# Kernel tuning notes

Measured on AMD Instinct MI355X. Metric: run time of the kernel, lower is better.

The kernel has to match this reference:

```python
import jax, jax.numpy as jnp
import numpy as np

B, S, D = 8, 512, 512
H = 8
DPH = D // H
FFN = 2048
N_LAYERS = 4
K = 2048 * 8  # vocab_size * vq_vocab_size_factor
COMMIT = 0.25
LN_EPS = 1e-5
# replicates torch bug: scale = key.size(-1)//num_heads AFTER head split view
SCALE = DPH // H  # 64 // 8 = 8, attention is MULTIPLIED by this


def setup_inputs():
    key = jax.random.key(0)
    ks = jax.random.split(key, 12)
    init = lambda k, shape, s=0.02: (jax.random.normal(k, shape, jnp.float32) * s)
    inp = {
        'vec_inputs': jax.random.normal(ks[0], (B, S, D), jnp.float32),
        'Wq': init(ks[1], (N_LAYERS, D, D)), 'bq': jnp.zeros((N_LAYERS, D)),
        'Wk': init(ks[2], (N_LAYERS, D, D)), 'bk': jnp.zeros((N_LAYERS, D)),
        'Wv': init(ks[3], (N_LAYERS, D, D)), 'bv': jnp.zeros((N_LAYERS, D)),
        'Wo': init(ks[4], (N_LAYERS, D, D)), 'bo': jnp.zeros((N_LAYERS, D)),
        'ln1_g': jnp.ones((N_LAYERS, D)), 'ln1_b': jnp.zeros((N_LAYERS, D)),
        'W1': init(ks[5], (N_LAYERS, D, FFN)), 'b1': jnp.zeros((N_LAYERS, FFN)),
        'W2': init(ks[6], (N_LAYERS, FFN, D)), 'b2': jnp.zeros((N_LAYERS, D)),
        'ln2_g': jnp.ones((N_LAYERS, D)), 'ln2_b': jnp.zeros((N_LAYERS, D)),
        # VectorQuantizerEMA: embedding.weight.data.normal_()
        'codebook': jax.random.normal(ks[7], (K, D), jnp.float32),
    }
    return inp


def _layernorm(x, g, b):
    mu = jnp.mean(x, axis=-1, keepdims=True)
    var = jnp.mean((x - mu) ** 2, axis=-1, keepdims=True)
    return (x - mu) * jax.lax.rsqrt(var + LN_EPS) * g + b


def _encoder_layer(x, Wq, bq, Wk, bk, Wv, bv, Wo, bo, ln1_g, ln1_b, W1, b1, W2, b2, ln2_g, ln2_b):
    resid = x
    q = x @ Wq + bq  # [B,S,D]
    k = x @ Wk + bk
    v = x @ Wv + bv
    # faithful to torch .view(B*H, -1, dph): raw row-major reshape (NOT transpose split)
    q = q.reshape(B * H, S, DPH)
    k = k.reshape(B * H, S, DPH)
    v = v.reshape(B * H, S, DPH)
    att = jnp.einsum('bqd,bkd->bqk', q, k) * SCALE
    att = jax.nn.softmax(att, axis=-1)
    ctx = jnp.einsum('bqk,bkd->bqd', att, v).reshape(B, S, D)
    out = ctx @ Wo + bo
    out = _layernorm(resid + out, ln1_g, ln1_b)
    # position-wise FFN (Conv1d kernel 1 == Linear)
    ff = jax.nn.relu(out @ W1 + b1) @ W2 + b2
    out = _layernorm(out + ff, ln2_g, ln2_b)
    return out


def reference(vec_inputs, Wq, bq, Wk, bk, Wv, bv, Wo, bo, ln1_g, ln1_b,
              W1, b1, W2, b2, ln2_g, ln2_b, codebook):
    ze = vec_inputs
    for l in range(N_LAYERS):
        ze = _encoder_layer(ze, Wq[l], bq[l], Wk[l], bk[l], Wv[l], bv[l], Wo[l], bo[l],
                            ln1_g[l], ln1_b[l], W1[l], b1[l], W2[l], b2[l], ln2_g[l], ln2_b[l])
    # VectorQuantizerEMA forward (eval mode: no EMA updates)
    flat = ze.reshape(-1, D)  # [B*S, D]
    d = (jnp.sum(flat ** 2, axis=1, keepdims=True)
         + jnp.sum(codebook ** 2, axis=1)
         - 2.0 * flat @ codebook.T)  # [B*S, K]
    idx = jnp.argmin(d, axis=1)  # [B*S]
    quant = codebook[idx].reshape(ze.shape)
    e_latent = jnp.mean((jax.lax.stop_gradient(quant) - ze) ** 2)
    loss = COMMIT * e_latent
    zq = ze + jax.lax.stop_gradient(quant - ze)  # straight-through
    avg_probs = jnp.zeros((K,), jnp.float32).at[idx].add(1.0) / flat.shape[0]
    perplexity = jnp.exp(-jnp.sum(avg_probs * jnp.log(avg_probs + 1e-10)))
    return zq, idx.reshape(B, S), loss, perplexity
```

## Files before the change

### kernel.cpp

```cpp
#include <hip/hip_runtime.h>

#define MROWS 4096
#define DDIM  512
#define FFND  2048
#define NLAY  4
#define KCB   16384
#define LN_EPS 1e-5f

typedef unsigned short u16;
typedef _Float16 half8 __attribute__((ext_vector_type(8)));
typedef float f32x4 __attribute__((ext_vector_type(4)));

#define B_X    0ULL
#define B_Q    8388608ULL
#define B_K    16777216ULL
#define B_V    25165824ULL
#define B_CT   33554432ULL
#define B_TMP  41943040ULL
#define B_H    8388608ULL
#define B_CBH  8388608ULL
#define B_CBL  25165824ULL
#define B_ZEH  41943040ULL
#define B_ZEL  46137344ULL
#define B_ZN   50331648ULL
#define B_CN   50348032ULL
#define B_RL   50413568ULL
#define B_BEST 50429952ULL
#define B_HIST 50462720ULL
#define B_WT   50528256ULL

__device__ __forceinline__ void splitf16(float x, u16& h, u16& l) {
  _Float16 hh = (_Float16)x;
  float r = x - (float)hh;
  _Float16 ll = (_Float16)r;
  h = *(u16*)&hh; l = *(u16*)&ll;
}

__device__ __forceinline__ unsigned int fkey(float f) {
  unsigned int u = __float_as_uint(f);
  return (u & 0x80000000u) ? ~u : (u | 0x80000000u);
}

template<int EPI>
__device__ __forceinline__ void gemm64_body(const float* __restrict__ Af,
    const u16* __restrict__ Bhi, const u16* __restrict__ Blo,
    const float* __restrict__ bias, float* __restrict__ C, int Kd, int N) {
  __shared__ __align__(16) u16 As[2][2048];
  __shared__ __align__(16) u16 Bs[2][4096];
  const int t = threadIdx.x;
  const int w = t >> 6, l = t & 63;
  const int lr = l & 15, lg = l >> 4;
  const int m0 = blockIdx.y * 64, n0 = blockIdx.x * 128;

  f32x4 acc[4][2];
  const f32x4 zf = {0.f, 0.f, 0.f, 0.f};
#pragma unroll
  for (int mi = 0; mi < 4; ++mi)
#pragma unroll
    for (int ni = 0; ni < 2; ++ni) acc[mi][ni] = zf;

  for (int k0 = 0; k0 < Kd; k0 += 32) {
#pragma unroll
    for (int pl = 0; pl < 2; ++pl) {
      const u16* gp = pl ? Blo : Bhi;
      u16* lb = &Bs[pl][0];
#pragma unroll
      for (int i = 0; i < 2; ++i) {
        int ob = w * 2048 + i * 1024;
        int o = ob + l * 16;
        int r = o >> 6;
        int pc = (o >> 4) & 3;
        int c = pc ^ ((r + (r >> 2)) & 3);
        const u16* g = gp + (size_t)(n0 + r) * Kd + k0 + c * 8;
        __builtin_amdgcn_global_load_lds(
            (const __attribute__((address_space(1))) unsigned int*)(const void*)g,
            (__attribute__((address_space(3))) unsigned int*)(void*)(lb + (ob >> 1)), 16, 0, 0);
      }
    }
#pragma unroll
    for (int p = 0; p < 2; ++p) {
      int e = p * 256 + t;
      int r = e >> 3, kc = (e & 7) * 4;
      float4 a = *(const float4*)(Af + (size_t)(m0 + r) * Kd + k0 + kc);
      u16 h0, h1, h2, h3, q0, q1, q2, q3;
      splitf16(a.x, h0, q0); splitf16(a.y, h1, q1); splitf16(a.z, h2, q2); splitf16(a.w, h3, q3);
      int idx = r * 32 + ((((kc >> 3) ^ ((r + (r >> 2)) & 3))) << 3) + (kc & 7);
      *(uint2*)&As[0][idx] = make_uint2((unsigned)h0 | ((unsigned)h1 << 16), (unsigned)h2 | ((unsigned)h3 << 16));
      *(uint2*)&As[1][idx] = make_uint2((unsigned)q0 | ((unsigned)q1 << 16), (unsigned)q2 | ((unsigned)q3 << 16));
    }
    __syncthreads();
    half8 ah[4], al[4], bh2[2], bl2[2];
#pragma unroll
    for (int mi = 0; mi < 4; ++mi) {
      int r = mi * 16 + lr;
      int idx = r * 32 + ((lg ^ ((r + (r >> 2)) & 3)) << 3);
      ah[mi] = *(const half8*)&As[0][idx];
      al[mi] = *(const half8*)&As[1][idx];
    }
#pragma unroll
    for (int ni = 0; ni < 2; ++ni) {
      int r = w * 32 + ni * 16 + lr;
      int idx = r * 32 + ((lg ^ ((r + (r >> 2)) & 3)) << 3);
      bh2[ni] = *(const half8*)&Bs[0][idx];
      bl2[ni] = *(const half8*)&Bs[1][idx];
    }
#pragma unroll
    for (int mi = 0; mi < 4; ++mi)
#pragma unroll
      for (int ni = 0; ni < 2; ++ni) {
        acc[mi][ni] = __builtin_amdgcn_mfma_f32_16x16x32_f16(ah[mi], bh2[ni], acc[mi][ni], 0, 0, 0);
        acc[mi][ni] = __builtin_amdgcn_mfma_f32_16x16x32_f16(ah[mi], bl2[ni], acc[mi][ni], 0, 0, 0);
        acc[mi][ni] = __builtin_amdgcn_mfma_f32_16x16x32_f16(al[mi], bh2[ni], acc[mi][ni], 0, 0, 0);
      }
    __syncthreads();
  }

  float bv[2];
#pragma unroll
  for (int ni = 0; ni < 2; ++ni) bv[ni] = bias[n0 + w * 32 + ni * 16 + lr];
#pragma unroll
  for (int mi = 0; mi < 4; ++mi)
#pragma unroll
    for (int j = 0; j < 4; ++j) {
      int m = m0 + mi * 16 + lg * 4 + j;
#pragma unroll
      for (int ni = 0; ni < 2; ++ni) {
        int n = n0 + w * 32 + ni * 16 + lr;
        float o = acc[mi][ni][j] + bv[ni];
        if (EPI == 1) o = fmaxf(o, 0.f);
        C[(size_t)m * N + n] = o;
      }
    }
}

__global__ __launch_bounds__(256) void qkv_enc(const float* __restrict__ Af,
    const u16* __restrict__ wt, const float* __restrict__ bq, const float* __restrict__ bk,
    const float* __restrict__ bv_, float* __restrict__ Cq) {
  const int z = blockIdx.z;
  const u16* Bhi = wt + (size_t)z * 524288;
  const u16* Blo = Bhi + 262144;
  const float* bias = (z == 0) ? bq : (z == 1) ? bk : bv_;
  float* C = Cq + (size_t)z * 2097152;
  gemm64_body<0>(Af, Bhi, Blo, bias, C, 512, 512);
}

__global__ __launch_bounds__(256) void gemm_enc(const float* __restrict__ Af,
    const u16* __restrict__ Bhi, const u16* __restrict__ Blo,
    const float* __restrict__ bias, float* __restrict__ C, int Kd, int N) {
  gemm64_body<0>(Af, Bhi, Blo, bias, C, Kd, N);
}

template<int EPI>
__global__ __launch_bounds__(256) void gemm128(const float* __restrict__ Af,
    const u16* __restrict__ Bhi, const u16* __restrict__ Blo,
    const float* __restrict__ bias, float* __restrict__ C, int Kd, int N) {
  __shared__ __align__(16) u16 As[2][4096];
  __shared__ __align__(16) u16 Bs[2][4096];
  const int t = threadIdx.x;
  const int w = t >> 6, l = t & 63;
  const int lr = l & 15, lg = l >> 4;
  const int wr = w >> 1, wc = w & 1;
  const int m0 = blockIdx.y * 128, n0 = blockIdx.x * 128;

  f32x4 acc[4][4];
  const f32x4 zf = {0.f, 0.f, 0.f, 0.f};
#pragma unroll
  for (int mi = 0; mi < 4; ++mi)
#pragma unroll
    for (int ni = 0; ni < 4; ++ni) acc[mi][ni] = zf;

  for (int k0 = 0; k0 < Kd; k0 += 32) {
#pragma unroll
    for (int pl = 0; pl < 2; ++pl) {
      const u16* gp = pl ? Blo : Bhi;
      u16* lb = &Bs[pl][0];
#pragma unroll
      for (int i = 0; i < 2; ++i) {
        int ob = (w * 2 + i) * 1024;
        int o = ob + l * 16;
        int r = o >> 6;
        int c = ((o >> 4) & 3) ^ ((r + (r >> 2)) & 3);
        const u16* g = gp + (size_t)(n0 + r) * Kd + k0 + c * 8;
        __builtin_amdgcn_global_load_lds(
            (const __attribute__((address_space(1))) unsigned int*)(const void*)g,
            (__attribute__((address_space(3))) unsigned int*)(void*)(lb + (ob >> 1)), 16, 0, 0);
      }
    }
#pragma unroll
    for (int p = 0; p < 4; ++p) {
      int e = p * 256 + t;
      int r = e >> 3, kc = (e & 7) * 4;
      float4 a = *(const float4*)(Af + (size_t)(m0 + r) * Kd + k0 + kc);
      u16 h0, h1, h2, h3, q0, q1, q2, q3;
      splitf16(a.x, h0, q0); splitf16(a.y, h1, q1); splitf16(a.z, h2, q2); splitf16(a.w, h3, q3);
      int idx = r * 32 + ((((kc >> 3) ^ ((r + (r >> 2)) & 3))) << 3) + (kc & 7);
      *(uint2*)&As[0][idx] = make_uint2((unsigned)h0 | ((unsigned)h1 << 16), (unsigned)h2 | ((unsigned)h3 << 16));
      *(uint2*)&As[1][idx] = make_uint2((unsigned)q0 | ((unsigned)q1 << 16), (unsigned)q2 | ((unsigned)q3 << 16));
    }
    __syncthreads();
    half8 ah[4], al[4], bh4[4], bl4[4];
#pragma unroll
    for (int mi = 0; mi < 4; ++mi) {
      int r = wr * 64 + mi * 16 + lr;
      int idx = r * 32 + ((lg ^ ((r + (r >> 2)) & 3)) << 3);
      ah[mi] = *(const half8*)&As[0][idx];
      al[mi] = *(const half8*)&As[1][idx];
    }
#pragma unroll
    for (int ni = 0; ni < 4; ++ni) {
      int r = wc * 64 + ni * 16 + lr;
      int idx = r * 32 + ((lg ^ ((r + (r >> 2)) & 3)) << 3);
      bh4[ni] = *(const half8*)&Bs[0][idx];
      bl4[ni] = *(const half8*)&Bs[1][idx];
    }
#pragma unroll
    for (int mi = 0; mi < 4; ++mi)
#pragma unroll
      for (int ni = 0; ni < 4; ++ni) {
        acc[mi][ni] = __builtin_amdgcn_mfma_f32_16x16x32_f16(ah[mi], bh4[ni], acc[mi][ni], 0, 0, 0);
        acc[mi][ni] = __builtin_amdgcn_mfma_f32_16x16x32_f16(ah[mi], bl4[ni], acc[mi][ni], 0, 0, 0);
        acc[mi][ni] = __builtin_amdgcn_mfma_f32_16x16x32_f16(al[mi], bh4[ni], acc[mi][ni], 0, 0, 0);
      }
    __syncthreads();
  }

  float bv[4];
#pragma unroll
  for (int ni = 0; ni < 4; ++ni) bv[ni] = bias[n0 + wc * 64 + ni * 16 + lr];
#pragma unroll
  for (int mi = 0; mi < 4; ++mi)
#pragma unroll
    for (int j = 0; j < 4; ++j) {
      int m = m0 + wr * 64 + mi * 16 + lg * 4 + j;
#pragma unroll
      for (int ni = 0; ni < 4; ++ni) {
        int n = n0 + wc * 64 + ni * 16 + lr;
        float o = acc[mi][ni][j] + bv[ni];
        if (EPI == 1) o = fmaxf(o, 0.f);
        C[(size_t)m * N + n] = o;
      }
    }
}

__global__ __launch_bounds__(512) void attn_mfma(const float* __restrict__ Q,
    const float* __restrict__ Kx, const float* __restrict__ V, float* __restrict__ O) {
  __shared__ __align__(16) u16 Ks[2][4608];
  __shared__ __align__(16) u16 Ps[2][9216];
  __shared__ __align__(16) u16 Vt[2][4608];
  const int t = threadIdx.x;
  const int w = t >> 6, l = t & 63;
  const int lr = l & 15, lg = l >> 4;
  const int bh = blockIdx.y;
  const int q0 = blockIdx.x * 128;
  const float* Qb = Q + ((size_t)bh * 512 + q0) * 64;
  const float* Kb = Kx + (size_t)bh * 512 * 64;
  const float* Vb = V + (size_t)bh * 512 * 64;

  const int srow = t >> 4, sc4 = (t & 15) * 4;

  half8 qh[2], qlo[2];
#pragma unroll
  for (int ks = 0; ks < 2; ++ks) {
    const float* p = Qb + (size_t)(w * 16 + lr) * 64 + ks * 32 + lg * 8;
    float4 f0 = *(const float4*)p;
    float4 f1 = *(const float4*)(p + 4);
    float v8[8] = {f0.x, f0.y, f0.z, f0.w, f1.x, f1.y, f1.z, f1.w};
#pragma unroll
    for (int j = 0; j < 8; ++j) {
      _Float16 hh = (_Float16)v8[j];
      float r = v8[j] - (float)hh;
      qh[ks][j] = hh;
      qlo[ks][j] = (_Float16)r;
    }
  }

  float mrun[4] = {-1e30f, -1e30f, -1e30f, -1e30f};
  float lrun[4] = {0.f, 0.f, 0.f, 0.f};
  f32x4 o[4];
  const f32x4 zf = {0.f, 0.f, 0.f, 0.f};
#pragma unroll
  for (int dn = 0; dn < 4; ++dn) o[dn] = zf;

  float4 kreg[2], vreg[2];
#pragma unroll
  for (int i = 0; i < 2; ++i) {
    int row = i * 32 + srow;
    kreg[i] = *(const float4*)(Kb + (size_t)row * 64 + sc4);
    vreg[i] = *(const float4*)(Vb + (size_t)row * 64 + sc4);
  }

#pragma unroll 1
  for (int kc = 0; kc < 8; ++kc) {
    __syncthreads();
#pragma unroll
    for (int i = 0; i < 2; ++i) {
      int row = i * 32 + srow;
      u16 h0, h1, h2, h3, l0, l1, l2, l3;
      splitf16(kreg[i].x, h0, l0); splitf16(kreg[i].y, h1, l1);
      splitf16(kreg[i].z, h2, l2); splitf16(kreg[i].w, h3, l3);
      *(uint2*)&Ks[0][row * 72 + sc4] = make_uint2((unsigned)h0 | ((unsigned)h1 << 16), (unsigned)h2 | ((unsigned)h3 << 16));
      *(uint2*)&Ks[1][row * 72 + sc4] = make_uint2((unsigned)l0 | ((unsigned)l1 << 16), (unsigned)l2 | ((unsigned)l3 << 16));
      u16 vh[4], vl[4];
      splitf16(vreg[i].x, vh[0], vl[0]); splitf16(vreg[i].y, vh[1], vl[1]);
      splitf16(vreg[i].z, vh[2], vl[2]); splitf16(vreg[i].w, vh[3], vl[3]);
#pragma unroll
      for (int ii = 0; ii < 4; ++ii) {
        Vt[0][(sc4 + ii) * 72 + row] = vh[ii];
        Vt[1][(sc4 + ii) * 72 + row] = vl[ii];
      }
    }
    __syncthreads();
    if (kc < 7) {
#pragma unroll
      for (int i = 0; i < 2; ++i) {
        int row = i * 32 + srow;
        kreg[i] = *(const float4*)(Kb + (size_t)((kc + 1) * 64 + row) * 64 + sc4);
        vreg[i] = *(const float4*)(Vb + (size_t)((kc + 1) * 64 + row) * 64 + sc4);
      }
    }
    f32x4 sa[4];
#pragma unroll
    for (int ni = 0; ni < 4; ++ni) sa[ni] = zf;
    __builtin_amdgcn_s_setprio(1);
#pragma unroll
    for (int ks = 0; ks < 2; ++ks) {
#pragma unroll
      for (int ni = 0; ni < 4; ++ni) {
        half8 kh = *(const half8*)&Ks[0][(ni * 16 + lr) * 72 + ks * 32 + lg * 8];
        half8 klo = *(const half8*)&Ks[1][(ni * 16 + lr) * 72 + ks * 32 + lg * 8];
        sa[ni] = __builtin_amdgcn_mfma_f32_16x16x32_f16(qh[ks], kh, sa[ni], 0, 0, 0);
        sa[ni] = __builtin_amdgcn_mfma_f32_16x16x32_f16(qh[ks], klo, sa[ni], 0, 0, 0);
        sa[ni] = __builtin_amdgcn_mfma_f32_16x16x32_f16(qlo[ks], kh, sa[ni], 0, 0, 0);
      }
    }
    __builtin_amdgcn_s_setprio(0);
#pragma unroll
    for (int j = 0; j < 4; ++j) {
      float sv[4];
#pragma unroll
      for (int ni = 0; ni < 4; ++ni) sv[ni] = sa[ni][j] * 8.f;
      float mx = fmaxf(fmaxf(sv[0], sv[1]), fmaxf(sv[2], sv[3]));
#pragma unroll
      for (int off = 8; off; off >>= 1) mx = fmaxf(mx, __shfl_xor(mx, off, 16));
      float mnew = fmaxf(mrun[j], mx);
      float fac = expf(mrun[j] - mnew);
      float ps = 0.f;
#pragma unroll
      for (int ni = 0; ni < 4; ++ni) {
        float p = expf(sv[ni] - mnew);
        ps += p;
        u16 ph_, pl_;
        splitf16(p, ph_, pl_);
        Ps[0][(w * 16 + lg * 4 + j) * 72 + ni * 16 + lr] = ph_;
        Ps[1][(w * 16 + lg * 4 + j) * 72 + ni * 16 + lr] = pl_;
      }
#pragma unroll
      for (int off = 8; off; off >>= 1) ps += __shfl_xor(ps, off, 16);
      lrun[j] = lrun[j] * fac + ps;
      mrun[j] = mnew;
#pragma unroll
      for (int dn = 0; dn < 4; ++dn) o[dn][j] *= fac;
    }
    __builtin_amdgcn_s_setprio(1);
#pragma unroll
    for (int ks = 0; ks < 2; ++ks) {
      half8 ph8 = *(const half8*)&Ps[0][(w * 16 + lr) * 72 + ks * 32 + lg * 8];
      half8 pl8 = *(const half8*)&Ps[1][(w * 16 + lr) * 72 + ks * 32 + lg * 8];
#pragma unroll
      for (int dn = 0; dn < 4; ++dn) {
        half8 vh8 = *(const half8*)&Vt[0][(dn * 16 + lr) * 72 + ks * 32 + lg * 8];
        half8 vl8 = *(const half8*)&Vt[1][(dn * 16 + lr) * 72 + ks * 32 + lg * 8];
        o[dn] = __builtin_amdgcn_mfma_f32_16x16x32_f16(ph8, vh8, o[dn], 0, 0, 0);
        o[dn] = __builtin_amdgcn_mfma_f32_16x16x32_f16(ph8, vl8, o[dn], 0, 0, 0);
        o[dn] = __builtin_amdgcn_mfma_f32_16x16x32_f16(pl8, vh8, o[dn], 0, 0, 0);
      }
    }
    __builtin_amdgcn_s_setprio(0);
  }
  float inv[4];
#pragma unroll
  for (int j = 0; j < 4; ++j) inv[j] = 1.f / lrun[j];
  float* Ob = O + ((size_t)bh * 512 + q0) * 64;
#pragma unroll
  for (int dn = 0; dn < 4; ++dn)
#pragma unroll
    for (int j = 0; j < 4; ++j)
      Ob[(size_t)(w * 16 + lg * 4 + j) * 64 + dn * 16 + lr] = o[dn][j] * inv[j];
}

__global__ __launch_bounds__(1024) void vq256(
    const u16* __restrict__ Ahi, const u16* __restrict__ Alo,
    const u16* __restrict__ Bhi, const u16* __restrict__ Blo,
    const float* __restrict__ zn, const float* __restrict__ cn,
    unsigned long long* __restrict__ best) {
  __shared__ __align__(16) u16 As[2][2][8192];
  __shared__ __align__(16) u16 Bs[2][2][8192];
  const int t = threadIdx.x;
  const int w = t >> 6, l = t & 63;
  const int lr = l & 15, lg = l >> 4;
  const int wr = w >> 2, wc = w & 3;
  const int f = blockIdx.x;
  const int xcd = f & 7, pos = f >> 3;
  const int ml = pos & 15;
  const int nl = pos >> 4;
  const int n0 = (xcd * 8 + nl) * 256;
  const int m0 = ml * 256;

  f32x4 acc[4][4];
  const f32x4 zf = {0.f, 0.f, 0.f, 0.f};
#pragma unroll
  for (int mi = 0; mi < 4; ++mi)
#pragma unroll
    for (int ni = 0; ni < 4; ++ni) acc[mi][ni] = zf;

  const int s_ob = w * 1024;
  int s_r, s_c;
  {
    int o = s_ob + l * 16;
    s_r = o >> 6;
    s_c = ((o >> 4) & 3) ^ ((s_r + (s_r >> 2)) & 3);
  }

#define VQ_STAGE(buf, k0)                                                               \
  {                                                                                     \
    size_t ea = (size_t)(m0 + s_r) * 512 + (k0) + s_c * 8;                              \
    size_t eb = (size_t)(n0 + s_r) * 512 + (k0) + s_c * 8;                              \
    __builtin_amdgcn_global_load_lds(                                                   \
        (const __attribute__((address_space(1))) unsigned int*)(const void*)(Ahi + ea), \
        (__attribute__((address_space(3))) unsigned int*)(void*)(&As[buf][0][s_ob >> 1]), 16, 0, 0); \
    __builtin_amdgcn_global_load_lds(                                                   \
        (const __attribute__((address_space(1))) unsigned int*)(const void*)(Alo + ea), \
        (__attribute__((address_space(3))) unsigned int*)(void*)(&As[buf][1][s_ob >> 1]), 16, 0, 0); \
    __builtin_amdgcn_global_load_lds(                                                   \
        (const __attribute__((address_space(1))) unsigned int*)(const void*)(Bhi + eb), \
        (__attribute__((address_space(3))) unsigned int*)(void*)(&Bs[buf][0][s_ob >> 1]), 16, 0, 0); \
    __builtin_amdgcn_global_load_lds(                                                   \
        (const __attribute__((address_space(1))) unsigned int*)(const void*)(Blo + eb), \
        (__attribute__((address_space(3))) unsigned int*)(void*)(&Bs[buf][1][s_ob >> 1]), 16, 0, 0); \
  }

#define VQ_COMPUTE(buf)                                                                 \
  {                                                                                     \
    half8 bh[4], bl[4];                                                                 \
    _Pragma("unroll")                                                                   \
    for (int ni = 0; ni < 4; ++ni) {                                                    \
      int r = wc * 64 + ni * 16 + lr;                                                   \
      int idx = r * 32 + ((lg ^ ((r + (r >> 2)) & 3)) << 3);                            \
      bh[ni] = *(const half8*)&Bs[buf][0][idx];                                         \
      bl[ni] = *(const half8*)&Bs[buf][1][idx];                                         \
    }                                                                                   \
    _Pragma("unroll")                                                                   \
    for (int mi = 0; mi < 4; ++mi) {                                                    \
      int r = wr * 64 + mi * 16 + lr;                                                   \
      int idx = r * 32 + ((lg ^ ((r + (r >> 2)) & 3)) << 3);                            \
      half8 ah = *(const half8*)&As[buf][0][idx];                                       \
      half8 al = *(const half8*)&As[buf][1][idx];                                       \
      _Pragma("unroll")                                                                 \
      for (int ni = 0; ni < 4; ++ni) {                                                  \
        acc[mi][ni] = __builtin_amdgcn_mfma_f32_16x16x32_f16(ah, bh[ni], acc[mi][ni], 0, 0, 0); \
        acc[mi][ni] = __builtin_amdgcn_mfma_f32_16x16x32_f16(ah, bl[ni], acc[mi][ni], 0, 0, 0); \
        acc[mi][ni] = __builtin_amdgcn_mfma_f32_16x16x32_f16(al, bh[ni], acc[mi][ni], 0, 0, 0); \
      }                                                                                 \
    }                                                                                   \
  }

  VQ_STAGE(0, 0);
  asm volatile("s_waitcnt vmcnt(0)" ::: "memory");
  __builtin_amdgcn_s_barrier();
  int cur = 0;
#pragma unroll 1
  for (int ks = 0; ks < 16; ++ks) {
    if (ks < 15) VQ_STAGE(cur ^ 1, (ks + 1) * 32);
    VQ_COMPUTE(cur);
    asm volatile("s_waitcnt vmcnt(0)" ::: "memory");
    __builtin_amdgcn_s_barrier();
    cur ^= 1;
  }

  float cnv[4];
#pragma unroll
  for (int ni = 0; ni < 4; ++ni) cnv[ni] = cn[n0 + wc * 64 + ni * 16 + lr];
#pragma unroll
  for (int mi = 0; mi < 4; ++mi)
#pragma unroll
    for (int j = 0; j < 4; ++j) {
      int m = m0 + wr * 64 + mi * 16 + lg * 4 + j;
      float zr = zn[m];
      float db = 3.4e38f; int jb = 0;
#pragma unroll
      for (int ni = 0; ni < 4; ++ni) {
        float dd = zr + cnv[ni] - 2.f * acc[mi][ni][j];
        int nn = n0 + wc * 64 + ni * 16 + lr;
        if (dd < db) { db = dd; jb = nn; }
      }
      unsigned long long key = ((unsigned long long)fkey(db) << 32) | (unsigned int)jb;
#pragma unroll
      for (int off = 8; off; off >>= 1) {
        unsigned long long o = __shfl_xor(key, off, 16);
        if (o < key) key = o;
      }
      if (lr == 0) atomicMin(best + m, key);
    }
#undef VQ_STAGE
#undef VQ_COMPUTE
}

__global__ __launch_bounds__(256) void wcvt_layer(const float* __restrict__ Wq,
    const float* __restrict__ Wk, const float* __restrict__ Wv, const float* __restrict__ Wo,
    const float* __restrict__ W1, const float* __restrict__ W2, u16* __restrict__ wt) {
  __shared__ float Ls[64][68];
  const int T = blockIdx.x, t = threadIdx.x;
  const float* src; u16 *dh, *dl; int K, N, kt, nt;
  if (T < 256) {
    int mat = T >> 6, tt = T & 63;
    src = (mat == 0) ? Wq : (mat == 1) ? Wk : (mat == 2) ? Wv : Wo;
    dh = wt + (size_t)mat * 524288; dl = dh + 262144;
    K = 512; N = 512; kt = tt >> 3; nt = tt & 7;
  } else if (T < 512) {
    int tt = T - 256; src = W1; dh = wt + 2097152; dl = dh + 1048576;
    K = 512; N = 2048; kt = tt >> 5; nt = tt & 31;
  } else {
    int tt = T - 512; src = W2; dh = wt + 4194304; dl = dh + 1048576;
    K = 2048; N = 512; kt = tt >> 3; nt = tt & 7;
  }
  const int k0 = kt * 64, n0 = nt * 64;
#pragma unroll
  for (int p = 0; p < 4; ++p) {
    int e = p * 256 + t;
    int kr = e >> 4, nc = (e & 15) * 4;
    *(float4*)&Ls[kr][nc] = *(const float4*)(src + (size_t)(k0 + kr) * N + n0 + nc);
  }
  __syncthreads();
  {
    int n = t >> 2, kc = (t & 3) * 16;
    unsigned hw[8], lw[8];
#pragma unroll
    for (int i = 0; i < 8; ++i) {
      u16 ha, la, hb, lb;
      splitf16(Ls[kc + 2 * i][n], ha, la);
      splitf16(Ls[kc + 2 * i + 1][n], hb, lb);
      hw[i] = (unsigned)ha | ((unsigned)hb << 16);
      lw[i] = (unsigned)la | ((unsigned)lb << 16);
    }
    size_t o = (size_t)(n0 + n) * K + k0 + kc;
    *(uint4*)&dh[o] = make_uint4(hw[0], hw[1], hw[2], hw[3]);
    *(uint4*)&dh[o + 8] = make_uint4(hw[4], hw[5], hw[6], hw[7]);
    *(uint4*)&dl[o] = make_uint4(lw[0], lw[1], lw[2], lw[3]);
    *(uint4*)&dl[o + 8] = make_uint4(lw[4], lw[5], lw[6], lw[7]);
  }
}

__global__ __launch_bounds__(128) void zcvt_kernel(const float* __restrict__ src,
    u16* __restrict__ hi, u16* __restrict__ lo, float* __restrict__ nrm) {
  __shared__ float red[2];
  const int row = blockIdx.x, t = threadIdx.x;
  const float4 a = *(const float4*)(src + (size_t)row * 512 + t * 4);
  u16 h0, h1, h2, h3, q0, q1, q2, q3;
  splitf16(a.x, h0, q0); splitf16(a.y, h1, q1); splitf16(a.z, h2, q2); splitf16(a.w, h3, q3);
  *(uint2*)&hi[(size_t)row * 512 + t * 4] = make_uint2((unsigned)h0 | ((unsigned)h1 << 16), (unsigned)h2 | ((unsigned)h3 << 16));
  *(uint2*)&lo[(size_t)row * 512 + t * 4] = make_uint2((unsigned)q0 | ((unsigned)q1 << 16), (unsigned)q2 | ((unsigned)q3 << 16));
  float s = a.x * a.x + a.y * a.y + a.z * a.z + a.w * a.w;
#pragma unroll
  for (int off = 32; off; off >>= 1) s += __shfl_xor(s, off, 64);
  if ((t & 63) == 0) red[t >> 6] = s;
  __syncthreads();
  if (t == 0) nrm[row] = red[0] + red[1];
}

__global__ __launch_bounds__(128) void ln_kernel(const float* __restrict__ A,
    const float* __restrict__ Dl, const float* __restrict__ g,
    const float* __restrict__ bb, float* __restrict__ out) {
  __shared__ float red[2];
  const int row = blockIdx.x, t = threadIdx.x;
  const float4 a = *(const float4*)(A + (size_t)row * 512 + t * 4);
  const float4 d = *(const float4*)(Dl + (size_t)row * 512 + t * 4);
  float v0 = a.x + d.x, v1 = a.y + d.y, v2 = a.z + d.z, v3 = a.w + d.w;
  float s = v0 + v1 + v2 + v3;
#pragma unroll
  for (int off = 32; off; off >>= 1) s += __shfl_xor(s, off, 64);
  if ((t & 63) == 0) red[t >> 6] = s;
  __syncthreads();
  const float mu = (red[0] + red[1]) * (1.f / 512.f);
  const float w0 = v0 - mu, w1 = v1 - mu, w2 = v2 - mu, w3 = v3 - mu;
  float q = w0 * w0 + w1 * w1 + w2 * w2 + w3 * w3;
  __syncthreads();
#pragma unroll
  for (int off = 32; off; off >>= 1) q += __shfl_xor(q, off, 64);
  if ((t & 63) == 0) red[t >> 6] = q;
  __syncthreads();
  const float rs = rsqrtf((red[0] + red[1]) * (1.f / 512.f) + LN_EPS);
  const float4 gv = *(const float4*)(g + t * 4);
  const float4 bv = *(const float4*)(bb + t * 4);
  *(float4*)(out + (size_t)row * 512 + t * 4) =
      make_float4(w0 * rs * gv.x + bv.x, w1 * rs * gv.y + bv.y, w2 * rs * gv.z + bv.z, w3 * rs * gv.w + bv.w);
}

__global__ __launch_bounds__(128) void gather_kernel(const unsigned long long* __restrict__ best,
    const float* __restrict__ Cb, const float* __restrict__ Ze, float* __restrict__ zq,
    float* __restrict__ oidx, float* __restrict__ rloss, int* __restrict__ hist) {
  __shared__ float red[2];
  const int row = blockIdx.x, t = threadIdx.x;
  const int idx = (int)(best[row] & 0xFFFFFFFFULL);
  const float4 c = *(const float4*)(Cb + (size_t)idx * 512 + t * 4);
  const float4 z = *(const float4*)(Ze + (size_t)row * 512 + t * 4);
  *(float4*)(zq + (size_t)row * 512 + t * 4) = c;
  const float d0 = c.x - z.x, d1 = c.y - z.y, d2 = c.z - z.z, d3 = c.w - z.w;
  float s = d0 * d0 + d1 * d1 + d2 * d2 + d3 * d3;
#pragma unroll
  for (int off = 32; off; off >>= 1) s += __shfl_xor(s, off, 64);
  if ((t & 63) == 0) red[t >> 6] = s;
  __syncthreads();
  if (t == 0) {
    rloss[row] = red[0] + red[1];
    oidx[row] = (float)idx;
    atomicAdd(hist + idx, 1);
  }
}

__global__ __launch_bounds__(256) void fin_kernel(const float* __restrict__ rloss,
    const int* __restrict__ hist, float* __restrict__ oloss, float* __restrict__ oppl) {
  __shared__ float red[4];
  const int t = threadIdx.x;
  float s = 0.f;
  for (int i = t; i < 4096; i += 256) s += rloss[i];
#pragma unroll
  for (int off = 32; off; off >>= 1) s += __shfl_xor(s, off, 64);
  if ((t & 63) == 0) red[t >> 6] = s;
  __syncthreads();
  if (t == 0) oloss[0] = 0.25f * (red[0] + red[1] + red[2] + red[3]) * (1.f / 2097152.f);
  float e = 0.f;
  for (int i = t; i < KCB; i += 256) {
    float p = (float)hist[i] * (1.f / 4096.f);
    e += p * logf(p + 1e-10f);
  }
#pragma unroll
  for (int off = 32; off; off >>= 1) e += __shfl_xor(e, off, 64);
  __syncthreads();
  if ((t & 63) == 0) red[t >> 6] = e;
  __syncthreads();
  if (t == 0) oppl[0] = expf(-(red[0] + red[1] + red[2] + red[3]));
}

extern "C" void kernel_launch(void* const* d_in, const int* in_sizes, int n_in,
                              void* d_out, int out_size, void* d_ws, size_t ws_size,
                              hipStream_t stream) {
  const float* vec  = (const float*)d_in[0];
  const float* Wq   = (const float*)d_in[1];
  const float* bq   = (const float*)d_in[2];
  const float* Wk   = (const float*)d_in[3];
  const float* bk   = (const float*)d_in[4];
  const float* Wv   = (const float*)d_in[5];
  const float* bv   = (const float*)d_in[6];
  const float* Wo   = (const float*)d_in[7];
  const float* bo   = (const float*)d_in[8];
  const float* l1g  = (const float*)d_in[9];
  const float* l1b  = (const float*)d_in[10];
  const float* W1   = (const float*)d_in[11];
  const float* b1   = (const float*)d_in[12];
  const float* W2   = (const float*)d_in[13];
  const float* b2   = (const float*)d_in[14];
  const float* l2g  = (const float*)d_in[15];
  const float* l2b  = (const float*)d_in[16];
  const float* cb   = (const float*)d_in[17];

  char* wsb = (char*)d_ws;
  float* x   = (float*)(wsb + B_X);
  float* q   = (float*)(wsb + B_Q);
  float* k   = (float*)(wsb + B_K);
  float* v   = (float*)(wsb + B_V);
  float* ctx = (float*)(wsb + B_CT);
  float* tmp = (float*)(wsb + B_TMP);
  float* h   = (float*)(wsb + B_H);
  u16* cbh = (u16*)(wsb + B_CBH);
  u16* cbl = (u16*)(wsb + B_CBL);
  u16* zeh = (u16*)(wsb + B_ZEH);
  u16* zel = (u16*)(wsb + B_ZEL);
  float* zn = (float*)(wsb + B_ZN);
  float* cn = (float*)(wsb + B_CN);
  float* rl = (float*)(wsb + B_RL);
  unsigned long long* best = (unsigned long long*)(wsb + B_BEST);
  int* hist = (int*)(wsb + B_HIST);
  u16* wt = (u16*)(wsb + B_WT);
  u16* wto_h = wt + 1572864;      u16* wto_l = wt + 1835008;
  u16* wt1_h = wt + 2097152;      u16* wt1_l = wt + 3145728;
  u16* wt2_h = wt + 4194304;      u16* wt2_l = wt + 5242880;

  float* zq   = (float*)d_out;
  float* oidx = (float*)d_out + 2097152;
  float* olos = (float*)d_out + 2097152 + 4096;
  float* oppl = olos + 1;

  const dim3 gQkv(4, 64, 3);
  const dim3 gProj(4, 64);
  const dim3 gFfn1(16, 32);
  const dim3 gAttn(4, 64);

  for (int l = 0; l < NLAY; ++l) {
    const float* xin = l ? (const float*)x : vec;
    const size_t wo = (size_t)l * DDIM * DDIM;
    wcvt_layer<<<768, 256, 0, stream>>>(Wq + wo, Wk + wo, Wv + wo, Wo + wo,
        W1 + (size_t)l * DDIM * FFND, W2 + (size_t)l * FFND * DDIM, wt);
    qkv_enc<<<gQkv, 256, 0, stream>>>(xin, wt, bq + l * DDIM, bk + l * DDIM, bv + l * DDIM, q);
    attn_mfma<<<gAttn, 512, 0, stream>>>(q, k, v, ctx);
    gemm_enc<<<gProj, 256, 0, stream>>>(ctx, wto_h, wto_l, bo + l * DDIM, tmp, DDIM, DDIM);
    ln_kernel<<<MROWS, 128, 0, stream>>>(xin, tmp, l1g + l * DDIM, l1b + l * DDIM, x);
    gemm128<1><<<gFfn1, 256, 0, stream>>>(x, wt1_h, wt1_l, b1 + l * FFND, h, DDIM, FFND);
    gemm_enc<<<gProj, 256, 0, stream>>>(h, wt2_h, wt2_l, b2 + l * DDIM, tmp, FFND, DDIM);
    ln_kernel<<<MROWS, 128, 0, stream>>>(x, tmp, l2g + l * DDIM, l2b + l * DDIM, x);
  }

  zcvt_kernel<<<MROWS, 128, 0, stream>>>(x, zeh, zel, zn);
  zcvt_kernel<<<KCB, 128, 0, stream>>>(cb, cbh, cbl, cn);
  hipMemsetAsync(best, 0xFF, 4096 * 8, stream);
  hipMemsetAsync(hist, 0, KCB * 4, stream);
  vq256<<<1024, 1024, 0, stream>>>(zeh, zel, cbh, cbl, zn, cn, best);
  gather_kernel<<<MROWS, 128, 0, stream>>>(best, cb, x, zq, oidx, rl, hist);
  fin_kernel<<<1, 256, 0, stream>>>(rl, hist, olos, oppl);
}
```

Baseline: 1.033 ms.

## Split-K the output and FFN2 projections and fold partial sums into layernorm

Replaces the single-pass 64x128-tile projection GEMMs (Wo and W2) with a split-K variant that launches twice as many blocks, each covering half the reduction dimension and writing its own partial buffer. The layernorm kernel now reads both partials plus the bias and sums them with the residual, so no separate reduction pass is needed. This raises block count for the 512-wide outputs to improve CU occupancy, at the cost of an extra full-size fp32 write and read per GEMM.

Result: faster. 901.8 us (median of 2 runs) (-12.7%).

```diff
diff --git a/kernel.cpp b/kernel.cpp
--- a/kernel.cpp
+++ b/kernel.cpp
@@ -28,6 +28,7 @@
 #define B_BEST 50429952ULL
 #define B_HIST 50462720ULL
 #define B_WT   50528256ULL
+#define B_TMP2 63111168ULL
 
 __device__ __forceinline__ void splitf16(float x, u16& h, u16& l) {
   _Float16 hh = (_Float16)x;
@@ -144,10 +145,94 @@
   gemm64_body<0>(Af, Bhi, Blo, bias, C, 512, 512);
 }
 
-__global__ __launch_bounds__(256) void gemm_enc(const float* __restrict__ Af,
+__global__ __launch_bounds__(256) void gemm_splitk(const float* __restrict__ Af,
     const u16* __restrict__ Bhi, const u16* __restrict__ Blo,
-    const float* __restrict__ bias, float* __restrict__ C, int Kd, int N) {
-  gemm64_body<0>(Af, Bhi, Blo, bias, C, Kd, N);
+    float* __restrict__ C0, float* __restrict__ C1, int Kd, int N) {
+  __shared__ __align__(16) u16 As[2][2048];
+  __shared__ __align__(16) u16 Bs[2][4096];
+  const int t = threadIdx.x;
+  const int w = t >> 6, l = t & 63;
+  const int lr = l & 15, lg = l >> 4;
+  const int m0 = blockIdx.y * 64, n0 = blockIdx.x * 128;
+  const int z = blockIdx.z;
+  const int koff = z * (Kd >> 1);
+  const int kend = koff + (Kd >> 1);
+  float* C = z ? C1 : C0;
+
+  f32x4 acc[4][2];
+  const f32x4 zf = {0.f, 0.f, 0.f, 0.f};
+#pragma unroll
+  for (int mi = 0; mi < 4; ++mi)
+#pragma unroll
+    for (int ni = 0; ni < 2; ++ni) acc[mi][ni] = zf;
+
+  for (int k0 = koff; k0 < kend; k0 += 32) {
+#pragma unroll
+    for (int pl = 0; pl < 2; ++pl) {
+      const u16* gp = pl ? Blo : Bhi;
+      u16* lb = &Bs[pl][0];
+#pragma unroll
+      for (int i = 0; i < 2; ++i) {
+        int ob = w * 2048 + i * 1024;
+        int o = ob + l * 16;
+        int r = o >> 6;
+        int pc = (o >> 4) & 3;
+        int c = pc ^ ((r + (r >> 2)) & 3);
+        const u16* g = gp + (size_t)(n0 + r) * Kd + k0 + c * 8;
+        __builtin_amdgcn_global_load_lds(
+            (const __attribute__((address_space(1))) unsigned int*)(const void*)g,
+            (__attribute__((address_space(3))) unsigned int*)(void*)(lb + (ob >> 1)), 16, 0, 0);
+      }
+    }
+#pragma unroll
+    for (int p = 0; p < 2; ++p) {
+      int e = p * 256 + t;
+      int r = e >> 3, kc = (e & 7) * 4;
+      float4 a = *(const float4*)(Af + (size_t)(m0 + r) * Kd + k0 + kc);
+      u16 h0, h1, h2, h3, q0, q1, q2, q3;
+      splitf16(a.x, h0, q0); splitf16(a.y, h1, q1); splitf16(a.z, h2, q2); splitf16(a.w, h3, q3);
+      int idx = r * 32 + ((((kc >> 3) ^ ((r + (r >> 2)) & 3))) << 3) + (kc & 7);
+      *(uint2*)&As[0][idx] = make_uint2((unsigned)h0 | ((unsigned)h1 << 16), (unsigned)h2 | ((unsigned)h3 << 16));
+      *(uint2*)&As[1][idx] = make_uint2((unsigned)q0 | ((unsigned)q1 << 16), (unsigned)q2 | ((unsigned)q3 << 16));
+    }
+    __syncthreads();
+    half8 ah[4], al[4], bh2[2], bl2[2];
+#pragma unroll
+    for (int mi = 0; mi < 4; ++mi) {
+      int r = mi * 16 + lr;
+      int idx = r * 32 + ((lg ^ ((r + (r >> 2)) & 3)) << 3);
+      ah[mi] = *(const half8*)&As[0][idx];
+      al[mi] = *(const half8*)&As[1][idx];
+    }
+#pragma unroll
+    for (int ni = 0; ni < 2; ++ni) {
+      int r = w * 32 + ni * 16 + lr;
+      int idx = r * 32 + ((lg ^ ((r + (r >> 2)) & 3)) << 3);
+      bh2[ni] = *(const half8*)&Bs[0][idx];
+      bl2[ni] = *(const half8*)&Bs[1][idx];
+    }
+#pragma unroll
+    for (int mi = 0; mi < 4; ++mi)
+#pragma unroll
+      for (int ni = 0; ni < 2; ++ni) {
+        acc[mi][ni] = __builtin_amdgcn_mfma_f32_16x16x32_f16(ah[mi], bh2[ni], acc[mi][ni], 0, 0, 0);
+        acc[mi][ni] = __builtin_amdgcn_mfma_f32_16x16x32_f16(ah[mi], bl2[ni], acc[mi][ni], 0, 0, 0);
+        acc[mi][ni] = __builtin_amdgcn_mfma_f32_16x16x32_f16(al[mi], bh2[ni], acc[mi][ni], 0, 0, 0);
+      }
+    __syncthreads();
+  }
+
+#pragma unroll
+  for (int mi = 0; mi < 4; ++mi)
+#pragma unroll
+    for (int j = 0; j < 4; ++j) {
+      int m = m0 + mi * 16 + lg * 4 + j;
+#pragma unroll
+      for (int ni = 0; ni < 2; ++ni) {
+        int n = n0 + w * 32 + ni * 16 + lr;
+        C[(size_t)m * N + n] = acc[mi][ni][j];
+      }
+    }
 }
 
 template<int EPI>
@@ -567,14 +652,17 @@
   if (t == 0) nrm[row] = red[0] + red[1];
 }
 
-__global__ __launch_bounds__(128) void ln_kernel(const float* __restrict__ A,
-    const float* __restrict__ Dl, const float* __restrict__ g,
-    const float* __restrict__ bb, float* __restrict__ out) {
+__global__ __launch_bounds__(128) void ln3_kernel(const float* __restrict__ A,
+    const float* __restrict__ D1, const float* __restrict__ D2, const float* __restrict__ gb,
+    const float* __restrict__ g, const float* __restrict__ bb, float* __restrict__ out) {
   __shared__ float red[2];
   const int row = blockIdx.x, t = threadIdx.x;
-  const float4 a = *(const float4*)(A + (size_t)row * 512 + t * 4);
-  const float4 d = *(const float4*)(Dl + (size_t)row * 512 + t * 4);
-  float v0 = a.x + d.x, v1 = a.y + d.y, v2 = a.z + d.z, v3 = a.w + d.w;
+  const float4 a  = *(const float4*)(A  + (size_t)row * 512 + t * 4);
+  const float4 d1 = *(const float4*)(D1 + (size_t)row * 512 + t * 4);
+  const float4 d2 = *(const float4*)(D2 + (size_t)row * 512 + t * 4);
+  const float4 gv2 = *(const float4*)(gb + t * 4);
+  float v0 = a.x + d1.x + d2.x + gv2.x, v1 = a.y + d1.y + d2.y + gv2.y;
+  float v2 = a.z + d1.z + d2.z + gv2.z, v3 = a.w + d1.w + d2.w + gv2.w;
   float s = v0 + v1 + v2 + v3;
 #pragma unroll
   for (int off = 32; off; off >>= 1) s += __shfl_xor(s, off, 64);
@@ -664,13 +752,14 @@
   const float* cb   = (const float*)d_in[17];
 
   char* wsb = (char*)d_ws;
-  float* x   = (float*)(wsb + B_X);
-  float* q   = (float*)(wsb + B_Q);
-  float* k   = (float*)(wsb + B_K);
-  float* v   = (float*)(wsb + B_V);
-  float* ctx = (float*)(wsb + B_CT);
-  float* tmp = (float*)(wsb + B_TMP);
-  float* h   = (float*)(wsb + B_H);
+  float* x    = (float*)(wsb + B_X);
+  float* q    = (float*)(wsb + B_Q);
+  float* k    = (float*)(wsb + B_K);
+  float* v    = (float*)(wsb + B_V);
+  float* ctx  = (float*)(wsb + B_CT);
+  float* tmp  = (float*)(wsb + B_TMP);
+  float* tmp2 = (float*)(wsb + B_TMP2);
+  float* h    = (float*)(wsb + B_H);
   u16* cbh = (u16*)(wsb + B_CBH);
   u16* cbl = (u16*)(wsb + B_CBL);
   u16* zeh = (u16*)(wsb + B_ZEH);
@@ -691,7 +780,7 @@
   float* oppl = olos + 1;
 
   const dim3 gQkv(4, 64, 3);
-  const dim3 gProj(4, 64);
+  const dim3 gSplit(4, 64, 2);
   const dim3 gFfn1(16, 32);
   const dim3 gAttn(4, 64);
 
@@ -702,11 +791,13 @@
         W1 + (size_t)l * DDIM * FFND, W2 + (size_t)l * FFND * DDIM, wt);
     qkv_enc<<<gQkv, 256, 0, stream>>>(xin, wt, bq + l * DDIM, bk + l * DDIM, bv + l * DDIM, q);
     attn_mfma<<<gAttn, 512, 0, stream>>>(q, k, v, ctx);
-    gemm_enc<<<gProj, 256, 0, stream>>>(ctx, wto_h, wto_l, bo + l * DDIM, tmp, DDIM, DDIM);
-    ln_kernel<<<MROWS, 128, 0, stream>>>(xin, tmp, l1g + l * DDIM, l1b + l * DDIM, x);
+    gemm_splitk<<<gSplit, 256, 0, stream>>>(ctx, wto_h, wto_l, tmp, tmp2, DDIM, DDIM);
+    ln3_kernel<<<MROWS, 128, 0, stream>>>(xin, tmp, tmp2, bo + l * DDIM,
+        l1g + l * DDIM, l1b + l * DDIM, x);
     gemm128<1><<<gFfn1, 256, 0, stream>>>(x, wt1_h, wt1_l, b1 + l * FFND, h, DDIM, FFND);
-    gemm_enc<<<gProj, 256, 0, stream>>>(h, wt2_h, wt2_l, b2 + l * DDIM, tmp, FFND, DDIM);
-    ln_kernel<<<MROWS, 128, 0, stream>>>(x, tmp, l2g + l * DDIM, l2b + l * DDIM, x);
+    gemm_splitk<<<gSplit, 256, 0, stream>>>(h, wt2_h, wt2_l, tmp, tmp2, FFND, DDIM);
+    ln3_kernel<<<MROWS, 128, 0, stream>>>(x, tmp, tmp2, b2 + l * DDIM,
+        l2g + l * DDIM, l2b + l * DDIM, x);
   }
 
   zcvt_kernel<<<MROWS, 128, 0, stream>>>(x, zeh, zel, zn);
```

## Split-K the 512-wide GEMMs and fuse partial-sum reduction into consumers

Applied to the files above, without the earlier changes.

The QKV, output-projection and FFN2 GEMMs are split into two K-halves via blockIdx.z, doubling the number of blocks on the 64x128-tile launches. Each half writes its partial sums to its own buffer. The two partials plus the bias are summed inside the attention kernel (for Q/K/V) and inside a new LayerNorm variant (for the projections), so no separate reduction pass is needed. The aim is better CU occupancy on the small grids, paid for with extra partial-buffer writes and reads, and with the attention output aliasing the Q2 buffer.

Result: faster. 939.7 us (-9.0%).

```diff
diff --git a/kernel.cpp b/kernel.cpp
--- a/kernel.cpp
+++ b/kernel.cpp
@@ -28,6 +28,7 @@
 #define B_BEST 50429952ULL
 #define B_HIST 50462720ULL
 #define B_WT   50528256ULL
+#define B_TMP2 63111168ULL
 
 __device__ __forceinline__ void splitf16(float x, u16& h, u16& l) {
   _Float16 hh = (_Float16)x;
@@ -41,10 +42,9 @@
   return (u & 0x80000000u) ? ~u : (u | 0x80000000u);
 }
 
-template<int EPI>
-__device__ __forceinline__ void gemm64_body(const float* __restrict__ Af,
+__device__ __forceinline__ void gemm64_nk_body(const float* __restrict__ Af,
     const u16* __restrict__ Bhi, const u16* __restrict__ Blo,
-    const float* __restrict__ bias, float* __restrict__ C, int Kd, int N) {
+    float* __restrict__ C, int Kd, int N, int koff, int kend) {
   __shared__ __align__(16) u16 As[2][2048];
   __shared__ __align__(16) u16 Bs[2][4096];
   const int t = threadIdx.x;
@@ -59,7 +59,7 @@
 #pragma unroll
     for (int ni = 0; ni < 2; ++ni) acc[mi][ni] = zf;
 
-  for (int k0 = 0; k0 < Kd; k0 += 32) {
+  for (int k0 = koff; k0 < kend; k0 += 32) {
 #pragma unroll
     for (int pl = 0; pl < 2; ++pl) {
       const u16* gp = pl ? Blo : Bhi;
@@ -115,9 +115,6 @@
     __syncthreads();
   }
 
-  float bv[2];
-#pragma unroll
-  for (int ni = 0; ni < 2; ++ni) bv[ni] = bias[n0 + w * 32 + ni * 16 + lr];
 #pragma unroll
   for (int mi = 0; mi < 4; ++mi)
 #pragma unroll
@@ -126,28 +123,29 @@
 #pragma unroll
       for (int ni = 0; ni < 2; ++ni) {
         int n = n0 + w * 32 + ni * 16 + lr;
-        float o = acc[mi][ni][j] + bv[ni];
-        if (EPI == 1) o = fmaxf(o, 0.f);
-        C[(size_t)m * N + n] = o;
-      }
-    }
-}
-
-__global__ __launch_bounds__(256) void qkv_enc(const float* __restrict__ Af,
-    const u16* __restrict__ wt, const float* __restrict__ bq, const float* __restrict__ bk,
-    const float* __restrict__ bv_, float* __restrict__ Cq) {
+        C[(size_t)m * N + n] = acc[mi][ni][j];
+      }
+    }
+}
+
+__global__ __launch_bounds__(256) void gemm_splitk(const float* __restrict__ Af,
+    const u16* __restrict__ Bhi, const u16* __restrict__ Blo,
+    float* __restrict__ C0, float* __restrict__ C1, int Kd, int N) {
   const int z = blockIdx.z;
-  const u16* Bhi = wt + (size_t)z * 524288;
+  gemm64_nk_body(Af, Bhi, Blo, z ? C1 : C0, Kd, N, z * (Kd >> 1), (z + 1) * (Kd >> 1));
+}
+
+__global__ __launch_bounds__(256) void qkv_splitk(const float* __restrict__ Af,
+    const u16* __restrict__ wt,
+    float* __restrict__ q1, float* __restrict__ k1, float* __restrict__ v1,
+    float* __restrict__ q2, float* __restrict__ k2, float* __restrict__ v2) {
+  const int z = blockIdx.z;
+  const int mat = z >> 1, half = z & 1;
+  const u16* Bhi = wt + (size_t)mat * 524288;
   const u16* Blo = Bhi + 262144;
-  const float* bias = (z == 0) ? bq : (z == 1) ? bk : bv_;
-  float* C = Cq + (size_t)z * 2097152;
-  gemm64_body<0>(Af, Bhi, Blo, bias, C, 512, 512);
-}
-
-__global__ __launch_bounds__(256) void gemm_enc(const float* __restrict__ Af,
-    const u16* __restrict__ Bhi, const u16* __restrict__ Blo,
-    const float* __restrict__ bias, float* __restrict__ C, int Kd, int N) {
-  gemm64_body<0>(Af, Bhi, Blo, bias, C, Kd, N);
+  float* C = half ? ((mat == 0) ? q2 : (mat == 1) ? k2 : v2)
+                  : ((mat == 0) ? q1 : (mat == 1) ? k1 : v1);
+  gemm64_nk_body(Af, Bhi, Blo, C, 512, 512, half * 256, half * 256 + 256);
 }
 
 template<int EPI>
@@ -242,8 +240,12 @@
     }
 }
 
-__global__ __launch_bounds__(512) void attn_mfma(const float* __restrict__ Q,
-    const float* __restrict__ Kx, const float* __restrict__ V, float* __restrict__ O) {
+__global__ __launch_bounds__(512) void attn_mfma(
+    const float* __restrict__ Q1, const float* __restrict__ Q2,
+    const float* __restrict__ K1, const float* __restrict__ K2,
+    const float* __restrict__ V1, const float* __restrict__ V2,
+    const float* __restrict__ bq, const float* __restrict__ bk, const float* __restrict__ bv_,
+    float* __restrict__ O) {
   __shared__ __align__(16) u16 Ks[2][4608];
   __shared__ __align__(16) u16 Ps[2][9216];
   __shared__ __align__(16) u16 Vt[2][4608];
@@ -252,19 +254,32 @@
   const int lr = l & 15, lg = l >> 4;
   const int bh = blockIdx.y;
   const int q0 = blockIdx.x * 128;
-  const float* Qb = Q + ((size_t)bh * 512 + q0) * 64;
-  const float* Kb = Kx + (size_t)bh * 512 * 64;
-  const float* Vb = V + (size_t)bh * 512 * 64;
+  const size_t poff = ((size_t)bh * 512 + q0) * 64;
+  const size_t koffb = (size_t)bh * 512 * 64;
+  const float* Qb1 = Q1 + poff;
+  const float* Qb2 = Q2 + poff;
+  const float* Kb1 = K1 + koffb;
+  const float* Kb2 = K2 + koffb;
+  const float* Vb1 = V1 + koffb;
+  const float* Vb2 = V2 + koffb;
 
   const int srow = t >> 4, sc4 = (t & 15) * 4;
+  const float4 bk4 = *(const float4*)(bk + ((srow & 7) << 6) + sc4);
+  const float4 bv4 = *(const float4*)(bv_ + ((srow & 7) << 6) + sc4);
 
   half8 qh[2], qlo[2];
 #pragma unroll
   for (int ks = 0; ks < 2; ++ks) {
-    const float* p = Qb + (size_t)(w * 16 + lr) * 64 + ks * 32 + lg * 8;
-    float4 f0 = *(const float4*)p;
-    float4 f1 = *(const float4*)(p + 4);
-    float v8[8] = {f0.x, f0.y, f0.z, f0.w, f1.x, f1.y, f1.z, f1.w};
+    const size_t ro = (size_t)(w * 16 + lr) * 64 + ks * 32 + lg * 8;
+    float4 f0 = *(const float4*)(Qb1 + ro);
+    float4 f1 = *(const float4*)(Qb1 + ro + 4);
+    float4 g0 = *(const float4*)(Qb2 + ro);
+    float4 g1 = *(const float4*)(Qb2 + ro + 4);
+    const float* bp = bq + ((lr & 7) << 6) + ks * 32 + lg * 8;
+    float4 b0 = *(const float4*)bp;
+    float4 b1 = *(const float4*)(bp + 4);
+    float v8[8] = {f0.x + g0.x + b0.x, f0.y + g0.y + b0.y, f0.z + g0.z + b0.z, f0.w + g0.w + b0.w,
+                   f1.x + g1.x + b1.x, f1.y + g1.y + b1.y, f1.z + g1.z + b1.z, f1.w + g1.w + b1.w};
 #pragma unroll
     for (int j = 0; j < 8; ++j) {
       _Float16 hh = (_Float16)v8[j];
@@ -281,12 +296,14 @@
 #pragma unroll
   for (int dn = 0; dn < 4; ++dn) o[dn] = zf;
 
-  float4 kreg[2], vreg[2];
+  float4 kra[2], krb[2], vra[2], vrb[2];
 #pragma unroll
   for (int i = 0; i < 2; ++i) {
-    int row = i * 32 + srow;
-    kreg[i] = *(const float4*)(Kb + (size_t)row * 64 + sc4);
-    vreg[i] = *(const float4*)(Vb + (size_t)row * 64 + sc4);
+    size_t ro = (size_t)(i * 32 + srow) * 64 + sc4;
+    kra[i] = *(const float4*)(Kb1 + ro);
+    krb[i] = *(const float4*)(Kb2 + ro);
+    vra[i] = *(const float4*)(Vb1 + ro);
+    vrb[i] = *(const float4*)(Vb2 + ro);
   }
 
 #pragma unroll 1
@@ -295,14 +312,17 @@
 #pragma unroll
     for (int i = 0; i < 2; ++i) {
       int row = i * 32 + srow;
+      float kx = kra[i].x + krb[i].x + bk4.x, ky = kra[i].y + krb[i].y + bk4.y;
+      float kz = kra[i].z + krb[i].z + bk4.z, kw = kra[i].w + krb[i].w + bk4.w;
       u16 h0, h1, h2, h3, l0, l1, l2, l3;
-      splitf16(kreg[i].x, h0, l0); splitf16(kreg[i].y, h1, l1);
-      splitf16(kreg[i].z, h2, l2); splitf16(kreg[i].w, h3, l3);
+      splitf16(kx, h0, l0); splitf16(ky, h1, l1); splitf16(kz, h2, l2); splitf16(kw, h3, l3);
       *(uint2*)&Ks[0][row * 72 + sc4] = make_uint2((unsigned)h0 | ((unsigned)h1 << 16), (unsigned)h2 | ((unsigned)h3 << 16));
       *(uint2*)&Ks[1][row * 72 + sc4] = make_uint2((unsigned)l0 | ((unsigned)l1 << 16), (unsigned)l2 | ((unsigned)l3 << 16));
+      float vx = vra[i].x + vrb[i].x + bv4.x, vy = vra[i].y + vrb[i].y + bv4.y;
+      float vz = vra[i].z + vrb[i].z + bv4.z, vw = vra[i].w + vrb[i].w + bv4.w;
       u16 vh[4], vl[4];
-      splitf16(vreg[i].x, vh[0], vl[0]); splitf16(vreg[i].y, vh[1], vl[1]);
-      splitf16(vreg[i].z, vh[2], vl[2]); splitf16(vreg[i].w, vh[3], vl[3]);
+      splitf16(vx, vh[0], vl[0]); splitf16(vy, vh[1], vl[1]);
+      splitf16(vz, vh[2], vl[2]); splitf16(vw, vh[3], vl[3]);
 #pragma unroll
       for (int ii = 0; ii < 4; ++ii) {
         Vt[0][(sc4 + ii) * 72 + row] = vh[ii];
@@ -313,9 +333,11 @@
     if (kc < 7) {
 #pragma unroll
       for (int i = 0; i < 2; ++i) {
-        int row = i * 32 + srow;
-        kreg[i] = *(const float4*)(Kb + (size_t)((kc + 1) * 64 + row) * 64 + sc4);
-        vreg[i] = *(const float4*)(Vb + (size_t)((kc + 1) * 64 + row) * 64 + sc4);
+        size_t ro = (size_t)((kc + 1) * 64 + i * 32 + srow) * 64 + sc4;
+        kra[i] = *(const float4*)(Kb1 + ro);
+        krb[i] = *(const float4*)(Kb2 + ro);
+        vra[i] = *(const float4*)(Vb1 + ro);
+        vrb[i] = *(const float4*)(Vb2 + ro);
       }
     }
     f32x4 sa[4];
@@ -380,7 +402,7 @@
   float inv[4];
 #pragma unroll
   for (int j = 0; j < 4; ++j) inv[j] = 1.f / lrun[j];
-  float* Ob = O + ((size_t)bh * 512 + q0) * 64;
+  float* Ob = O + poff;
 #pragma unroll
   for (int dn = 0; dn < 4; ++dn)
 #pragma unroll
@@ -567,14 +589,17 @@
   if (t == 0) nrm[row] = red[0] + red[1];
 }
 
-__global__ __launch_bounds__(128) void ln_kernel(const float* __restrict__ A,
-    const float* __restrict__ Dl, const float* __restrict__ g,
-    const float* __restrict__ bb, float* __restrict__ out) {
+__global__ __launch_bounds__(128) void ln3_kernel(const float* __restrict__ A,
+    const float* __restrict__ D1, const float* __restrict__ D2, const float* __restrict__ gb,
+    const float* __restrict__ g, const float* __restrict__ bb, float* __restrict__ out) {
   __shared__ float red[2];
   const int row = blockIdx.x, t = threadIdx.x;
-  const float4 a = *(const float4*)(A + (size_t)row * 512 + t * 4);
-  const float4 d = *(const float4*)(Dl + (size_t)row * 512 + t * 4);
-  float v0 = a.x + d.x, v1 = a.y + d.y, v2 = a.z + d.z, v3 = a.w + d.w;
+  const float4 a  = *(const float4*)(A  + (size_t)row * 512 + t * 4);
+  const float4 d1 = *(const float4*)(D1 + (size_t)row * 512 + t * 4);
+  const float4 d2 = *(const float4*)(D2 + (size_t)row * 512 + t * 4);
+  const float4 gv2 = *(const float4*)(gb + t * 4);
+  float v0 = a.x + d1.x + d2.x + gv2.x, v1 = a.y + d1.y + d2.y + gv2.y;
+  float v2 = a.z + d1.z + d2.z + gv2.z, v3 = a.w + d1.w + d2.w + gv2.w;
   float s = v0 + v1 + v2 + v3;
 #pragma unroll
   for (int off = 32; off; off >>= 1) s += __shfl_xor(s, off, 64);
@@ -664,13 +689,14 @@
   const float* cb   = (const float*)d_in[17];
 
   char* wsb = (char*)d_ws;
-  float* x   = (float*)(wsb + B_X);
-  float* q   = (float*)(wsb + B_Q);
-  float* k   = (float*)(wsb + B_K);
-  float* v   = (float*)(wsb + B_V);
-  float* ctx = (float*)(wsb + B_CT);
-  float* tmp = (float*)(wsb + B_TMP);
-  float* h   = (float*)(wsb + B_H);
+  float* x    = (float*)(wsb + B_X);
+  float* q    = (float*)(wsb + B_Q);
+  float* k    = (float*)(wsb + B_K);
+  float* v    = (float*)(wsb + B_V);
+  float* ctx  = (float*)(wsb + B_CT);
+  float* tmp  = (float*)(wsb + B_TMP);
+  float* tmp2 = (float*)(wsb + B_TMP2);
+  float* h    = (float*)(wsb + B_H);
   u16* cbh = (u16*)(wsb + B_CBH);
   u16* cbl = (u16*)(wsb + B_CBL);
   u16* zeh = (u16*)(wsb + B_ZEH);
@@ -690,8 +716,8 @@
   float* olos = (float*)d_out + 2097152 + 4096;
   float* oppl = olos + 1;
 
-  const dim3 gQkv(4, 64, 3);
-  const dim3 gProj(4, 64);
+  const dim3 gQkv(4, 64, 6);
+  const dim3 gSplit(4, 64, 2);
   const dim3 gFfn1(16, 32);
   const dim3 gAttn(4, 64);
 
@@ -700,13 +726,16 @@
     const size_t wo = (size_t)l * DDIM * DDIM;
     wcvt_layer<<<768, 256, 0, stream>>>(Wq + wo, Wk + wo, Wv + wo, Wo + wo,
         W1 + (size_t)l * DDIM * FFND, W2 + (size_t)l * FFND * DDIM, wt);
-    qkv_enc<<<gQkv, 256, 0, stream>>>(xin, wt, bq + l * DDIM, bk + l * DDIM, bv + l * DDIM, q);
-    attn_mfma<<<gAttn, 512, 0, stream>>>(q, k, v, ctx);
-    gemm_enc<<<gProj, 256, 0, stream>>>(ctx, wto_h, wto_l, bo + l * DDIM, tmp, DDIM, DDIM);
-    ln_kernel<<<MROWS, 128, 0, stream>>>(xin, tmp, l1g + l * DDIM, l1b + l * DDIM, x);
+    qkv_splitk<<<gQkv, 256, 0, stream>>>(xin, wt, q, k, v, ctx, tmp, tmp2);
+    attn_mfma<<<gAttn, 512, 0, stream>>>(q, ctx, k, tmp, v, tmp2,
+        bq + l * DDIM, bk + l * DDIM, bv + l * DDIM, ctx);
+    gemm_splitk<<<gSplit, 256, 0, stream>>>(ctx, wto_h, wto_l, tmp, tmp2, DDIM, DDIM);
+    ln3_kernel<<<MROWS, 128, 0, stream>>>(xin, tmp, tmp2, bo + l * DDIM,
+        l1g + l * DDIM, l1b + l * DDIM, x);
     gemm128<1><<<gFfn1, 256, 0, stream>>>(x, wt1_h, wt1_l, b1 + l * FFND, h, DDIM, FFND);
-    gemm_enc<<<gProj, 256, 0, stream>>>(h, wt2_h, wt2_l, b2 + l * DDIM, tmp, FFND, DDIM);
-    ln_kernel<<<MROWS, 128, 0, stream>>>(x, tmp, l2g + l * DDIM, l2b + l * DDIM, x);
+    gemm_splitk<<<gSplit, 256, 0, stream>>>(h, wt2_h, wt2_l, tmp, tmp2, FFND, DDIM);
+    ln3_kernel<<<MROWS, 128, 0, stream>>>(x, tmp, tmp2, b2 + l * DDIM,
+        l2g + l * DDIM, l2b + l * DDIM, x);
   }
 
   zcvt_kernel<<<MROWS, 128, 0, stream>>>(x, zeh, zel, zn);
```
